# Performance work log

Measured on AMD Instinct MI355X. Metric: run time of the kernel, lower is better.

## Reference

```python
import jax, jax.numpy as jnp
import numpy as np

HIDDEN = 1024
N_HEADS = 16
N_LAYERS = 10
LOCAL_K = 3
TOKEN_T, TOKEN_H, TOKEN_W = 4, 16, 16
PATCH_SIZE = 2
LATENT_C = 16
TOKEN_DIM = LATENT_C * PATCH_SIZE * PATCH_SIZE  # 64
TOKEN_IN = TOKEN_DIM + 1                        # 65
N_TOKENS = TOKEN_T * TOKEN_H * TOKEN_W          # 1024
B = 1
HEAD_DIM = HIDDEN // N_HEADS
LN_EPS = 1e-5


def layer_norm(x, w, b):
    m = x.mean(-1, keepdims=True)
    v = ((x - m) ** 2).mean(-1, keepdims=True)
    return (x - m) * jax.lax.rsqrt(v + LN_EPS) * w + b


def patchify(lat):
    Bx, T, C, H, W = lat.shape
    ph, pw = H // PATCH_SIZE, W // PATCH_SIZE
    x = lat.reshape(Bx, T, C, ph, PATCH_SIZE, pw, PATCH_SIZE)
    x = x.transpose(0, 1, 3, 5, 2, 4, 6)
    return x.reshape(Bx, T * ph * pw, C * PATCH_SIZE * PATCH_SIZE)


def unpatchify(tok):
    Bx = tok.shape[0]
    C = TOKEN_DIM // (PATCH_SIZE * PATCH_SIZE)
    x = tok.reshape(Bx, TOKEN_T, TOKEN_H, TOKEN_W, C, PATCH_SIZE, PATCH_SIZE)
    x = x.transpose(0, 1, 4, 2, 5, 3, 6)
    return x.reshape(Bx, TOKEN_T, C, TOKEN_H * PATCH_SIZE, TOKEN_W * PATCH_SIZE)


def gather_neighbors(kv):
    # kv: (B, N, 2D) -> (B, N, 27, 2D), 3x3x3 zero-padded neighborhoods
    Bx, Nx, D2 = kv.shape
    pad = LOCAL_K // 2
    x = kv.reshape(Bx, TOKEN_T, TOKEN_H, TOKEN_W, D2)
    x = jnp.pad(x, ((0, 0), (pad, pad), (pad, pad), (pad, pad), (0, 0)))
    sl = [x[:, dt:dt + TOKEN_T, dh:dh + TOKEN_H, dw:dw + TOKEN_W]
          for dt in range(LOCAL_K) for dh in range(LOCAL_K) for dw in range(LOCAL_K)]
    nb = jnp.stack(sl, axis=4)  # (B,T,H,W,27,2D)
    return nb.reshape(Bx, Nx, LOCAL_K ** 3, D2)


def local_attention(x, qkv_w, out_w):
    Bx, Nx, D = x.shape
    H, d = N_HEADS, HEAD_DIM
    qkv = x @ qkv_w                       # (B,N,3D)
    q, k, v = jnp.split(qkv, 3, axis=-1)
    kv_nb = gather_neighbors(jnp.concatenate([k, v], axis=-1))  # (B,N,27,2D)
    k_nb, v_nb = jnp.split(kv_nb, 2, axis=-1)
    q = q.reshape(Bx, Nx, H, d)
    k_nb = k_nb.reshape(Bx, Nx, LOCAL_K ** 3, H, d)
    v_nb = v_nb.reshape(Bx, Nx, LOCAL_K ** 3, H, d)
    scores = jnp.einsum('bnhd,bnkhd->bnhk', q, k_nb) / np.sqrt(d).astype(np.float32)
    probs = jax.nn.softmax(scores, axis=-1)
    out = jnp.einsum('bnhk,bnkhd->bnhd', probs, v_nb).reshape(Bx, Nx, D)
    return out @ out_w


def global_attention(x, mask_flat, qkv_w, out_w):
    # Each masked query attends to all N keys; math identical to the
    # gather/SDPA/scatter in the original (per-query attention is independent),
    # realized as full attention masked to zero at unmasked positions.
    Bx, Nx, D = x.shape
    H, d = N_HEADS, HEAD_DIM
    qkv = x @ qkv_w
    q, k, v = jnp.split(qkv, 3, axis=-1)
    q = q.reshape(Bx, Nx, H, d)
    k = k.reshape(Bx, Nx, H, d)
    v = v.reshape(Bx, Nx, H, d)
    scores = jnp.einsum('bqhd,bkhd->bhqk', q, k) / np.sqrt(d).astype(np.float32)
    probs = jax.nn.softmax(scores, axis=-1)
    out = jnp.einsum('bhqk,bkhd->bqhd', probs, v).reshape(Bx, Nx, D)
    out = out @ out_w
    return out * mask_flat[..., None].astype(out.dtype)


def setup_inputs() -> dict:
    key = jax.random.key(0)
    ks = jax.random.split(key, 24)
    s = 0.02
    L, D = N_LAYERS, HIDDEN
    inp = {
        'latents': jax.random.normal(ks[0], (B, TOKEN_T, LATENT_C, TOKEN_H * PATCH_SIZE, TOKEN_W * PATCH_SIZE), jnp.float32),
        'token_mask': jax.random.uniform(ks[1], (B, TOKEN_T, TOKEN_H, TOKEN_W)) < 0.1,
        'input_proj_w': jax.random.normal(ks[2], (TOKEN_IN, D), jnp.float32) * s,
        'input_proj_b': jnp.zeros((D,), jnp.float32),
        'emb_t': jax.random.normal(ks[3], (TOKEN_T, D), jnp.float32) * s,
        'emb_h': jax.random.normal(ks[4], (TOKEN_H, D), jnp.float32) * s,
        'emb_w': jax.random.normal(ks[5], (TOKEN_W, D), jnp.float32) * s,
        'ln_local_w': jnp.ones((L, D), jnp.float32),
        'ln_local_b': jnp.zeros((L, D), jnp.float32),
        'ln_global_w': jnp.ones((L, D), jnp.float32),
        'ln_global_b': jnp.zeros((L, D), jnp.float32),
        'ln_ffn_w': jnp.ones((L, D), jnp.float32),
        'ln_ffn_b': jnp.zeros((L, D), jnp.float32),
        'local_qkv_w': jax.random.normal(ks[6], (L, D, 3 * D), jnp.float32) * s,
        'local_out_w': jax.random.normal(ks[7], (L, D, D), jnp.float32) * s,
        'global_qkv_w': jax.random.normal(ks[8], (L, D, 3 * D), jnp.float32) * s,
        'global_out_w': jax.random.normal(ks[9], (L, D, D), jnp.float32) * s,
        'ffn_w1': jax.random.normal(ks[10], (L, D, 4 * D), jnp.float32) * s,
        'ffn_b1': jnp.zeros((L, 4 * D), jnp.float32),
        'ffn_w2': jax.random.normal(ks[11], (L, 4 * D, D), jnp.float32) * s,
        'ffn_b2': jnp.zeros((L, D), jnp.float32),
        'final_ln_w': jnp.ones((D,), jnp.float32),
        'final_ln_b': jnp.zeros((D,), jnp.float32),
        # original zero-inits output_proj; use small random so the test is non-trivial
        'out_proj_w': jax.random.normal(ks[12], (D, TOKEN_DIM), jnp.float32) * s,
        'out_proj_b': jnp.zeros((TOKEN_DIM,), jnp.float32),
    }
    return inp


def reference(latents, token_mask, input_proj_w, input_proj_b, emb_t, emb_h, emb_w,
              ln_local_w, ln_local_b, ln_global_w, ln_global_b, ln_ffn_w, ln_ffn_b,
              local_qkv_w, local_out_w, global_qkv_w, global_out_w,
              ffn_w1, ffn_b1, ffn_w2, ffn_b2, final_ln_w, final_ln_b,
              out_proj_w, out_proj_b):
    Bx = latents.shape[0]
    mask_flat = token_mask.reshape(Bx, -1)
    tokens = patchify(latents)                       # (B, N, TOKEN_DIM)
    flag = mask_flat[..., None].astype(tokens.dtype)
    x = jnp.concatenate([tokens, flag], axis=-1) @ input_proj_w + input_proj_b

    tt, hh, ww = jnp.meshgrid(jnp.arange(TOKEN_T), jnp.arange(TOKEN_H), jnp.arange(TOKEN_W), indexing='ij')
    pos = emb_t[tt.reshape(-1)] + emb_h[hh.reshape(-1)] + emb_w[ww.reshape(-1)]
    x = x + pos[None]

    for l in range(N_LAYERS):
        x = x + local_attention(layer_norm(x, ln_local_w[l], ln_local_b[l]), local_qkv_w[l], local_out_w[l])
        x = x + global_attention(layer_norm(x, ln_global_w[l], ln_global_b[l]), mask_flat, global_qkv_w[l], global_out_w[l])
        h = layer_norm(x, ln_ffn_w[l], ln_ffn_b[l])
        h = jax.nn.gelu(h @ ffn_w1[l] + ffn_b1[l], approximate=False) @ ffn_w2[l] + ffn_b2[l]
        x = x + h

    delta = layer_norm(x, final_ln_w, final_ln_b) @ out_proj_w + out_proj_b
    return unpatchify(tokens + delta)
```

## Files before the change

### kernel.cpp

```cpp
#include <hip/hip_runtime.h>
#include <hip/hip_bf16.h>
#include <math.h>

typedef __bf16 bf16;
typedef __bf16 bf16x8 __attribute__((ext_vector_type(8)));
typedef __bf16 bf16x4 __attribute__((ext_vector_type(4)));
typedef float  f32x4 __attribute__((ext_vector_type(4)));
typedef unsigned int u32x4 __attribute__((ext_vector_type(4)));

#define NTOK 1024
#define HID  1024
#define NL   10
#define QCMAX 256

#define EPI_F32   0
#define EPI_GELU  1
#define EPI_RESID 2
#define EPI_BF16  3

__global__ __launch_bounds__(256)
void wtransall_k(const float* __restrict__ lqkv, const float* __restrict__ lout,
                 const float* __restrict__ gqkv, const float* __restrict__ gout,
                 const float* __restrict__ w1,   const float* __restrict__ w2,
                 bf16* __restrict__ lqkvT, bf16* __restrict__ loutT,
                 bf16* __restrict__ gqkvT, bf16* __restrict__ goutT,
                 bf16* __restrict__ w1T,   bf16* __restrict__ w2T)
{
    __shared__ bf16 tile[64 * 64];
    const int b = blockIdx.x;
    const float* W; bf16* O; int K, N, ti;
    if      (b < 768)  { W = lqkv; O = lqkvT; K = 1024; N = 3072; ti = b; }
    else if (b < 1024) { W = lout; O = loutT; K = 1024; N = 1024; ti = b - 768; }
    else if (b < 1792) { W = gqkv; O = gqkvT; K = 1024; N = 3072; ti = b - 1024; }
    else if (b < 2048) { W = gout; O = goutT; K = 1024; N = 1024; ti = b - 1792; }
    else if (b < 3072) { W = w1;   O = w1T;   K = 1024; N = 4096; ti = b - 2048; }
    else               { W = w2;   O = w2T;   K = 4096; N = 1024; ti = b - 3072; }
    const int ntx = N >> 6;
    const int n0 = (ti % ntx) * 64, k0 = (ti / ntx) * 64;
    const long mofs = (long)blockIdx.z * K * N;
    const float* Ws = W + mofs;
    bf16* Wo = O + mofs;
    const int t = threadIdx.x;
    {
        const int r = t >> 2, cc = (t & 3) * 16;
        const int x = (r >> 3) & 7;
        const int g0 = cc >> 3;
        const float* src = Ws + (long)(k0 + r) * N + n0 + cc;
        f32x4 a0 = *(const f32x4*)(src);
        f32x4 a1 = *(const f32x4*)(src + 4);
        f32x4 a2 = *(const f32x4*)(src + 8);
        f32x4 a3 = *(const f32x4*)(src + 12);
        bf16x8 w0, w1v;
        w0[0]=(bf16)a0.x; w0[1]=(bf16)a0.y; w0[2]=(bf16)a0.z; w0[3]=(bf16)a0.w;
        w0[4]=(bf16)a1.x; w0[5]=(bf16)a1.y; w0[6]=(bf16)a1.z; w0[7]=(bf16)a1.w;
        w1v[0]=(bf16)a2.x; w1v[1]=(bf16)a2.y; w1v[2]=(bf16)a2.z; w1v[3]=(bf16)a2.w;
        w1v[4]=(bf16)a3.x; w1v[5]=(bf16)a3.y; w1v[6]=(bf16)a3.z; w1v[7]=(bf16)a3.w;
        *(bf16x8*)&tile[r * 64 + ((g0    ) ^ x) * 8] = w0;
        *(bf16x8*)&tile[r * 64 + ((g0 | 1) ^ x) * 8] = w1v;
    }
    __syncthreads();
    {
        const int n = t >> 2, kc = (t & 3) * 16;
        const int g = n >> 3, no = n & 7;
        bf16x8 o0, o1;
#pragma unroll
        for (int j = 0; j < 8; ++j) {
            int r0 = kc + j, r1 = kc + 8 + j;
            o0[j] = tile[r0 * 64 + ((g ^ ((r0 >> 3) & 7)) * 8) + no];
            o1[j] = tile[r1 * 64 + ((g ^ ((r1 >> 3) & 7)) * 8) + no];
        }
        bf16* dst = Wo + (long)(n0 + n) * K + k0 + kc;
        *(bf16x8*)dst = o0;
        *(bf16x8*)(dst + 8) = o1;
    }
}

template<int EPI, int BM, int BN, int KSPLIT>
__global__ __launch_bounds__(256)
void gemm_k(const bf16* __restrict__ A, int lda, long bsA,
            const bf16* __restrict__ Bt, int ldb, long bsB,
            void* __restrict__ Cv, int ldc, long bsC,
            const float* __restrict__ bias, int K)
{
    constexpr int WC  = (BM == 128) ? 2 : 4;
    constexpr int WTN = BN / WC;
    constexpr int NF  = WTN / 16;
    __shared__ bf16 Al[2][BM * 32];
    __shared__ bf16 Bl[2][BN * 32];

    const int t    = threadIdx.x;
    const int lane = t & 63;
    const int wv   = t >> 6;
    const int wr   = wv / WC, wc = wv % WC;
    const int lrow = lane & 15, lk = lane >> 4;
    const int n0   = blockIdx.x * BN;
    const int m0   = blockIdx.y * BM;
    const int ks   = (KSPLIT > 1) ? (blockIdx.z % KSPLIT) : 0;
    const int bz   = (KSPLIT > 1) ? (blockIdx.z / KSPLIT) : blockIdx.z;
    const int Kc   = K / KSPLIT;

    const bf16* Ab = A  + bsA * bz + (long)ks * Kc;
    const bf16* Bb = Bt + bsB * bz + (long)ks * Kc;

    f32x4 acc[4][NF];
#pragma unroll
    for (int m = 0; m < 4; ++m)
#pragma unroll
        for (int n = 0; n < NF; ++n) acc[m][n] = f32x4{0.f, 0.f, 0.f, 0.f};

    const int sr = t >> 2, sc = (t & 3) * 8;

    auto stage = [&](int buf, int kk) {
#pragma unroll
        for (int i = 0; i < BM / 64; ++i)
            __builtin_amdgcn_global_load_lds(
                (const __attribute__((address_space(1))) void*)(Ab + (long)(m0 + sr + i * 64) * lda + kk + sc),
                (__attribute__((address_space(3))) void*)(&Al[buf][i * 2048 + t * 8]), 16, 0, 0);
#pragma unroll
        for (int i = 0; i < BN / 64; ++i)
            __builtin_amdgcn_global_load_lds(
                (const __attribute__((address_space(1))) void*)(Bb + (long)(n0 + sr + i * 64) * ldb + kk + sc),
                (__attribute__((address_space(3))) void*)(&Bl[buf][i * 2048 + t * 8]), 16, 0, 0);
    };

    stage(0, 0);
    __syncthreads();
    int cur = 0;
    for (int k0 = 0; k0 < Kc; k0 += 32) {
        if (k0 + 32 < Kc) stage(cur ^ 1, k0 + 32);
        bf16x8 af[4], bfv[NF];
#pragma unroll
        for (int m = 0; m < 4; ++m)
            af[m] = *(const bf16x8*)&Al[cur][(wr * 64 + m * 16 + lrow) * 32 + lk * 8];
#pragma unroll
        for (int n = 0; n < NF; ++n)
            bfv[n] = *(const bf16x8*)&Bl[cur][(wc * WTN + n * 16 + lrow) * 32 + lk * 8];
#pragma unroll
        for (int m = 0; m < 4; ++m)
#pragma unroll
            for (int n = 0; n < NF; ++n)
                acc[m][n] = __builtin_amdgcn_mfma_f32_16x16x32_bf16(af[m], bfv[n], acc[m][n], 0, 0, 0);
        __syncthreads();
        cur ^= 1;
    }

    float* Cf = (float*)Cv + bsC * blockIdx.z;
    bf16*  Cb = (bf16*)Cv + bsC * blockIdx.z;
#pragma unroll
    for (int m = 0; m < 4; ++m)
#pragma unroll
        for (int n = 0; n < NF; ++n) {
            const int c = n0 + wc * WTN + n * 16 + lrow;
#pragma unroll
            for (int q = 0; q < 4; ++q) {
                const int r = m0 + wr * 64 + m * 16 + lk * 4 + q;
                const float v = acc[m][n][q];
                const long off = (long)r * ldc + c;
                if (EPI == EPI_F32)        Cf[off] = v;
                else if (EPI == EPI_BF16)  Cb[off] = (bf16)v;
                else if (EPI == EPI_RESID) Cf[off] += v;
                else {
                    float u = v + bias[c];
                    Cb[off] = (bf16)(0.5f * u * (1.f + erff(u * 0.70710678118654752f)));
                }
            }
        }
}

template<int NS, bool BIAS, bool SCATTER>
__global__ __launch_bounds__(256)
void ln_add_k(float* __restrict__ x, const float* __restrict__ parts, long pstride,
              const float* __restrict__ bias, const int* __restrict__ rmap,
              const float* __restrict__ w, const float* __restrict__ b,
              bf16* __restrict__ o)
{
    int row  = blockIdx.x * 4 + (threadIdx.x >> 6);
    int lane = threadIdx.x & 63;
    f32x4* xr = (f32x4*)(x + (long)row * HID) + lane * 4;
    f32x4 v[4];
#pragma unroll
    for (int i = 0; i < 4; ++i) v[i] = xr[i];

    if (NS > 0) {
        int prow = SCATTER ? rmap[row] : row;
        if (!SCATTER || prow >= 0) {
            const float* pp = parts + (long)prow * 1024 + lane * 16;
#pragma unroll
            for (int ksi = 0; ksi < NS; ++ksi) {
                const f32x4* q = (const f32x4*)(pp + (long)ksi * pstride);
#pragma unroll
                for (int i = 0; i < 4; ++i) v[i] += q[i];
            }
            if (BIAS) {
                const f32x4* bb = (const f32x4*)bias + lane * 4;
#pragma unroll
                for (int i = 0; i < 4; ++i) v[i] += bb[i];
            }
#pragma unroll
            for (int i = 0; i < 4; ++i) xr[i] = v[i];
        }
    }

    float s = 0.f;
#pragma unroll
    for (int i = 0; i < 4; ++i) s += v[i].x + v[i].y + v[i].z + v[i].w;
    for (int m = 32; m; m >>= 1) s += __shfl_xor(s, m);
    float mean = s * (1.f / 1024.f);
    f32x4 d[4];
    float ss = 0.f;
#pragma unroll
    for (int i = 0; i < 4; ++i) {
        d[i] = v[i] - mean;
        ss += d[i].x * d[i].x + d[i].y * d[i].y + d[i].z * d[i].z + d[i].w * d[i].w;
    }
    for (int m = 32; m; m >>= 1) ss += __shfl_xor(ss, m);
    float rs = rsqrtf(ss * (1.f / 1024.f) + 1e-5f);
    const f32x4* wp = (const f32x4*)w + lane * 4;
    const f32x4* bp = (const f32x4*)b + lane * 4;
    bf16x8 o0, o1;
#pragma unroll
    for (int i = 0; i < 4; ++i) {
        f32x4 wv = wp[i], bv = bp[i];
        f32x4 e;
        e.x = d[i].x * rs * wv.x + bv.x; e.y = d[i].y * rs * wv.y + bv.y;
        e.z = d[i].z * rs * wv.z + bv.z; e.w = d[i].w * rs * wv.w + bv.w;
        if (i < 2) { o0[i*4+0]=(bf16)e.x; o0[i*4+1]=(bf16)e.y; o0[i*4+2]=(bf16)e.z; o0[i*4+3]=(bf16)e.w; }
        else       { int k=(i-2)*4; o1[k+0]=(bf16)e.x; o1[k+1]=(bf16)e.y; o1[k+2]=(bf16)e.z; o1[k+3]=(bf16)e.w; }
    }
    bf16* op = o + (long)row * HID + lane * 16;
    *(bf16x8*)op = o0;
    *(bf16x8*)(op + 8) = o1;
}

__global__ __launch_bounds__(256)
void red4pv_k(const float* __restrict__ p, bf16* __restrict__ Oc)
{
    int i = blockIdx.x * 256 + threadIdx.x;
    int d4 = (i & 15) * 4;
    int r  = (i >> 4) & 255;
    int h  = i >> 12;
    const float* base = p + (long)(h * 4) * 16384 + r * 64 + d4;
    f32x4 s = *(const f32x4*)base;
    s += *(const f32x4*)(base + 16384);
    s += *(const f32x4*)(base + 32768);
    s += *(const f32x4*)(base + 49152);
    bf16x4 o;
    o[0] = (bf16)s.x; o[1] = (bf16)s.y; o[2] = (bf16)s.z; o[3] = (bf16)s.w;
    *(bf16x4*)(Oc + (long)r * 1024 + h * 64 + d4) = o;
}

__global__ __launch_bounds__(256)
void lattn_k(const bf16* __restrict__ qkv, bf16* __restrict__ ao)
{
    int w    = blockIdx.x * 4 + (threadIdx.x >> 6);
    int lane = threadIdx.x & 63;
    int n = w >> 4, h = w & 15;
    int tt = n >> 8, hh = (n >> 4) & 15, ww = n & 15;

    int nj = -1;
    float dotv = 0.f;
    if (lane < 27) {
        int dt = lane / 9 - 1, dh = (lane % 9) / 3 - 1, dw = lane % 3 - 1;
        int t2 = tt + dt, h2 = hh + dh, w2 = ww + dw;
        if (t2 >= 0 && t2 < 4 && h2 >= 0 && h2 < 16 && w2 >= 0 && w2 < 16)
            nj = (t2 << 8) | (h2 << 4) | w2;
    }
    if (nj >= 0) {
        const bf16x8* qp = (const bf16x8*)(qkv + (long)n * 3072 + h * 64);
        const bf16x8* kp = (const bf16x8*)(qkv + (long)nj * 3072 + 1024 + h * 64);
#pragma unroll
        for (int i = 0; i < 8; ++i) {
            bf16x8 q8 = qp[i], k8 = kp[i];
#pragma unroll
            for (int j = 0; j < 8; ++j) dotv += (float)q8[j] * (float)k8[j];
        }
    }
    float sc = (lane < 27) ? dotv * 0.125f : -3.0e38f;
    float mx = sc;
    for (int m = 32; m; m >>= 1) mx = fmaxf(mx, __shfl_xor(mx, m));
    float e = (lane < 27) ? __expf(sc - mx) : 0.f;
    float s = e;
    for (int m = 32; m; m >>= 1) s += __shfl_xor(s, m);
    float p = e / s;

    float acc = 0.f;
    for (int j = 0; j < 27; ++j) {
        float pj = __shfl(p, j);
        int  njj = __shfl(nj, j);
        if (njj >= 0) acc += pj * (float)qkv[(long)njj * 3072 + 2048 + h * 64 + lane];
    }
    ao[(long)n * 1024 + h * 64 + lane] = (bf16)acc;
}

__global__ void compact_k(const int* __restrict__ mask, int* __restrict__ qidx,
                          int* __restrict__ rmap)
{
    int lane = threadIdx.x;
    int total = 0;
    for (int base = 0; base < 1024; base += 64) {
        int m = (mask[base + lane] != 0) ? 1 : 0;
        unsigned long long bal = __ballot(m);
        int pos = total + (int)__popcll(bal & ((1ull << lane) - 1ull));
        int ok = (m && pos < QCMAX);
        if (ok) qidx[pos] = base + lane;
        rmap[base + lane] = ok ? pos : -1;
        total += (int)__popcll(bal);
    }
    for (int i = total + lane; i < QCMAX; i += 64) qidx[i] = -1;
}

__global__ __launch_bounds__(256)
void qkvbuild_k(const bf16* __restrict__ qkv, const int* __restrict__ qidx,
                bf16* __restrict__ Qc, bf16* __restrict__ Kh, bf16* __restrict__ Vt)
{
    __shared__ bf16 vt[64][72];
    const int h = blockIdx.y;
    const int t = threadIdx.x;
    if (blockIdx.x < 4) {
        const int r = blockIdx.x * 64 + (t >> 2), dc = (t & 3) * 16;
        const int q = qidx[r];
        bf16x8 o0, o1;
        if (q >= 0) {
            const bf16x8* src = (const bf16x8*)(qkv + (long)q * 3072 + h * 64 + dc);
            bf16x8 a = src[0], b = src[1];
#pragma unroll
            for (int j = 0; j < 8; ++j) {
                o0[j] = (bf16)((float)a[j] * 0.125f);
                o1[j] = (bf16)((float)b[j] * 0.125f);
            }
        } else {
#pragma unroll
            for (int j = 0; j < 8; ++j) { o0[j] = (bf16)0.f; o1[j] = (bf16)0.f; }
        }
        bf16* dst = Qc + (long)h * (QCMAX * 64) + (long)r * 64 + dc;
        *(bf16x8*)dst = o0;
        *(bf16x8*)(dst + 8) = o1;
        return;
    }
    const int k0 = (blockIdx.x - 4) * 64;
    {
        const int r = t >> 2, dc = (t & 3) * 16;
        const bf16x8* kp = (const bf16x8*)(qkv + (long)(k0 + r) * 3072 + 1024 + h * 64 + dc);
        const bf16x8* vp = (const bf16x8*)(qkv + (long)(k0 + r) * 3072 + 2048 + h * 64 + dc);
        bf16x8 k0v = kp[0], k1v = kp[1];
        bf16* kd = Kh + (long)h * (NTOK * 64) + (long)(k0 + r) * 64 + dc;
        *(bf16x8*)kd = k0v;
        *(bf16x8*)(kd + 8) = k1v;
        *(bf16x8*)&vt[r][dc]     = vp[0];
        *(bf16x8*)&vt[r][dc + 8] = vp[1];
    }
    __syncthreads();
    {
        const int d = t >> 2, kc = (t & 3) * 16;
        bf16x8 o0, o1;
#pragma unroll
        for (int j = 0; j < 8; ++j) { o0[j] = vt[kc + j][d]; o1[j] = vt[kc + 8 + j][d]; }
        bf16* dst = Vt + (long)h * (64 * NTOK) + (long)d * NTOK + k0 + kc;
        *(bf16x8*)dst = o0;
        *(bf16x8*)(dst + 8) = o1;
    }
}

__global__ __launch_bounds__(256)
void softmax_k(const float* __restrict__ S, bf16* __restrict__ P)
{
    int row  = blockIdx.x * 4 + (threadIdx.x >> 6);
    int lane = threadIdx.x & 63;
    const f32x4* sp = (const f32x4*)(S + (long)row * 1024) + lane * 4;
    f32x4 v[4];
#pragma unroll
    for (int i = 0; i < 4; ++i) v[i] = sp[i];
    float mx = -3.0e38f;
#pragma unroll
    for (int i = 0; i < 4; ++i)
        mx = fmaxf(mx, fmaxf(fmaxf(v[i].x, v[i].y), fmaxf(v[i].z, v[i].w)));
    for (int m = 32; m; m >>= 1) mx = fmaxf(mx, __shfl_xor(mx, m));
    f32x4 ev[4];
    float sum = 0.f;
#pragma unroll
    for (int i = 0; i < 4; ++i) {
        ev[i].x = __expf(v[i].x - mx); ev[i].y = __expf(v[i].y - mx);
        ev[i].z = __expf(v[i].z - mx); ev[i].w = __expf(v[i].w - mx);
        sum += ev[i].x + ev[i].y + ev[i].z + ev[i].w;
    }
    for (int m = 32; m; m >>= 1) sum += __shfl_xor(sum, m);
    float inv = 1.f / sum;
    bf16x8 o0, o1;
#pragma unroll
    for (int i = 0; i < 4; ++i) {
        f32x4 e = ev[i] * inv;
        if (i < 2) { o0[i*4+0]=(bf16)e.x; o0[i*4+1]=(bf16)e.y; o0[i*4+2]=(bf16)e.z; o0[i*4+3]=(bf16)e.w; }
        else       { int k=(i-2)*4; o1[k+0]=(bf16)e.x; o1[k+1]=(bf16)e.y; o1[k+2]=(bf16)e.z; o1[k+3]=(bf16)e.w; }
    }
    bf16* op = P + (long)row * 1024 + lane * 16;
    *(bf16x8*)op = o0;
    *(bf16x8*)(op + 8) = o1;
}

__global__ __launch_bounds__(256)
void prep_k(const float* __restrict__ lat, const int* __restrict__ mask,
            const float* __restrict__ Wi, const float* __restrict__ bi,
            const float* __restrict__ et, const float* __restrict__ eh,
            const float* __restrict__ ew,
            float* __restrict__ x, float* __restrict__ tokens)
{
    __shared__ float tl[16][65];
    int t = threadIdx.x;
    int n0 = blockIdx.x * 16;
    for (int idx = t; idx < 16 * 65; idx += 256) {
        int ti = idx / 65, d = idx % 65;
        int n = n0 + ti;
        int tt = n >> 8, hh = (n >> 4) & 15, wwi = n & 15;
        float v;
        if (d < 64) {
            int c = d >> 2, ph = (d >> 1) & 1, pw = d & 1;
            v = lat[(((long)tt * 16 + c) * 32 + hh * 2 + ph) * 32 + wwi * 2 + pw];
            tokens[(long)n * 64 + d] = v;
        } else {
            v = mask[n] ? 1.f : 0.f;
        }
        tl[ti][d] = v;
    }
    __syncthreads();
    f32x4 acc[16];
#pragma unroll
    for (int i = 0; i < 16; ++i) acc[i] = f32x4{0.f, 0.f, 0.f, 0.f};
    for (int d = 0; d < 65; ++d) {
        f32x4 wv = *(const f32x4*)(Wi + (long)d * 1024 + t * 4);
#pragma unroll
        for (int ti = 0; ti < 16; ++ti) acc[ti] += tl[ti][d] * wv;
    }
    f32x4 bb = *(const f32x4*)(bi + t * 4);
    for (int ti = 0; ti < 16; ++ti) {
        int n = n0 + ti;
        int tt = n >> 8, hh = (n >> 4) & 15, wwi = n & 15;
        f32x4 pos = *(const f32x4*)(et + (long)tt * 1024 + t * 4)
                  + *(const f32x4*)(eh + (long)hh * 1024 + t * 4)
                  + *(const f32x4*)(ew + (long)wwi * 1024 + t * 4);
        *(f32x4*)(x + (long)n * 1024 + t * 4) = acc[ti] + bb + pos;
    }
}

__global__ __launch_bounds__(256)
void final_k(const bf16* __restrict__ xn, const float* __restrict__ OW,
             const float* __restrict__ ob, const float* __restrict__ tokens,
             float* __restrict__ out)
{
    __shared__ bf16 xl[8][1024];
    __shared__ float part[4][8][64];
    int t = threadIdx.x;
    int n0 = blockIdx.x * 8;
    for (int i = t; i < 1024; i += 256)
        ((u32x4*)xl)[i] = ((const u32x4*)(xn + (long)n0 * 1024))[i];
    __syncthreads();
    int j = t & 63, s = t >> 6;
    float acc[8] = {0.f, 0.f, 0.f, 0.f, 0.f, 0.f, 0.f, 0.f};
    for (int k = s * 256; k < s * 256 + 256; ++k) {
        float w = OW[(long)k * 64 + j];
#pragma unroll
        for (int ti = 0; ti < 8; ++ti) acc[ti] += (float)xl[ti][k] * w;
    }
    for (int ti = 0; ti < 8; ++ti) part[s][ti][j] = acc[ti];
    __syncthreads();
    if (s == 0) {
        for (int ti = 0; ti < 8; ++ti) {
            int n = n0 + ti;
            float v = part[0][ti][j] + part[1][ti][j] + part[2][ti][j] + part[3][ti][j]
                    + ob[j] + tokens[(long)n * 64 + j];
            int tt = n >> 8, hh = (n >> 4) & 15, wwi = n & 15;
            int c = j >> 2, ph = (j >> 1) & 1, pw = j & 1;
            out[(((long)tt * 16 + c) * 32 + hh * 2 + ph) * 32 + wwi * 2 + pw] = v;
        }
    }
}

extern "C" void kernel_launch(void* const* d_in, const int* in_sizes, int n_in,
                              void* d_out, int out_size, void* d_ws, size_t ws_size,
                              hipStream_t stream)
{
    const float* latents = (const float*)d_in[0];
    const int*   mask    = (const int*)d_in[1];
    const float* ipw  = (const float*)d_in[2];
    const float* ipb  = (const float*)d_in[3];
    const float* et   = (const float*)d_in[4];
    const float* eh   = (const float*)d_in[5];
    const float* ew   = (const float*)d_in[6];
    const float* lnlw = (const float*)d_in[7];
    const float* lnlb = (const float*)d_in[8];
    const float* lngw = (const float*)d_in[9];
    const float* lngb = (const float*)d_in[10];
    const float* lnfw = (const float*)d_in[11];
    const float* lnfb = (const float*)d_in[12];
    const float* lqkv = (const float*)d_in[13];
    const float* lout = (const float*)d_in[14];
    const float* gqkv = (const float*)d_in[15];
    const float* gout = (const float*)d_in[16];
    const float* w1   = (const float*)d_in[17];
    const float* b1   = (const float*)d_in[18];
    const float* w2   = (const float*)d_in[19];
    const float* b2   = (const float*)d_in[20];
    const float* flw  = (const float*)d_in[21];
    const float* flb  = (const float*)d_in[22];
    const float* opw  = (const float*)d_in[23];
    const float* opb  = (const float*)d_in[24];

    char* p = (char*)d_ws;
    auto alloc = [&](size_t bytes) { char* r = p; p += (bytes + 255) & ~(size_t)255; return r; };
    float* x      = (float*)alloc((size_t)4 << 20);
    bf16*  xn     = (bf16*)alloc((size_t)2 << 20);
    bf16*  qkvb   = (bf16*)alloc((size_t)6 << 20);
    bf16*  ao     = (bf16*)alloc((size_t)2 << 20);
    bf16*  hbuf   = (bf16*)alloc((size_t)8 << 20);
    float* tokens = (float*)alloc((size_t)256 << 10);
    bf16*  Qc     = (bf16*)alloc((size_t)512 << 10);
    bf16*  Kh     = (bf16*)alloc((size_t)2 << 20);
    bf16*  Vt     = (bf16*)alloc((size_t)2 << 20);
    float* S      = (float*)alloc((size_t)16 << 20);
    bf16*  P      = (bf16*)alloc((size_t)8 << 20);
    bf16*  Oc     = (bf16*)alloc((size_t)512 << 10);
    int*   qidx   = (int*)alloc(4096);
    int*   rmap   = (int*)alloc(4096);
    float* goutp  = (float*)alloc((size_t)8 * 256 * 1024 * 4);
    float* pvp    = (float*)alloc((size_t)64 * 256 * 64 * 4);
    float* f2p    = (float*)alloc((size_t)4 * 1024 * 1024 * 4);
    bf16* lqkvT = (bf16*)alloc((size_t)10 * 3072 * 1024 * 2);
    bf16* loutT = (bf16*)alloc((size_t)10 * 1024 * 1024 * 2);
    bf16* gqkvT = (bf16*)alloc((size_t)10 * 3072 * 1024 * 2);
    bf16* goutT = (bf16*)alloc((size_t)10 * 1024 * 1024 * 2);
    bf16* w1T   = (bf16*)alloc((size_t)10 * 4096 * 1024 * 2);
    bf16* w2T   = (bf16*)alloc((size_t)10 * 1024 * 4096 * 2);

    wtransall_k<<<dim3(4096, 1, NL), 256, 0, stream>>>(
        lqkv, lout, gqkv, gout, w1, w2, lqkvT, loutT, gqkvT, goutT, w1T, w2T);

    prep_k<<<64, 256, 0, stream>>>(latents, mask, ipw, ipb, et, eh, ew, x, tokens);
    compact_k<<<1, 64, 0, stream>>>(mask, qidx, rmap);

    for (int l = 0; l < NL; ++l) {
        const long wq  = (long)l * 3072 * 1024;
        const long wo  = (long)l * 1024 * 1024;
        const long wf1 = (long)l * 4096 * 1024;

        if (l == 0)
            ln_add_k<0, false, false><<<256, 256, 0, stream>>>(
                x, nullptr, 0, nullptr, nullptr, lnlw, lnlb, xn);
        else
            ln_add_k<4, true, false><<<256, 256, 0, stream>>>(
                x, f2p, (long)1024 * 1024, b2 + (l - 1) * 1024, nullptr,
                lnlw + l * HID, lnlb + l * HID, xn);

        gemm_k<EPI_BF16, 64, 128, 1><<<dim3(24, 16, 1), 256, 0, stream>>>(
            xn, 1024, 0, lqkvT + wq, 1024, 0, qkvb, 3072, 0, nullptr, 1024);
        lattn_k<<<4096, 256, 0, stream>>>(qkvb, ao);
        gemm_k<EPI_RESID, 64, 128, 1><<<dim3(8, 16, 1), 256, 0, stream>>>(
            ao, 1024, 0, loutT + wo, 1024, 0, x, 1024, 0, nullptr, 1024);

        ln_add_k<0, false, false><<<256, 256, 0, stream>>>(
            x, nullptr, 0, nullptr, nullptr, lngw + l * HID, lngb + l * HID, xn);

        gemm_k<EPI_BF16, 64, 128, 1><<<dim3(24, 16, 1), 256, 0, stream>>>(
            xn, 1024, 0, gqkvT + wq, 1024, 0, qkvb, 3072, 0, nullptr, 1024);
        qkvbuild_k<<<dim3(20, 16), 256, 0, stream>>>(qkvb, qidx, Qc, Kh, Vt);
        gemm_k<EPI_F32, 64, 128, 1><<<dim3(8, 4, 16), 256, 0, stream>>>(
            Qc, 64, (long)256 * 64, Kh, 64, (long)1024 * 64,
            S, 1024, (long)256 * 1024, nullptr, 64);
        softmax_k<<<1024, 256, 0, stream>>>(S, P);
        gemm_k<EPI_F32, 64, 64, 4><<<dim3(1, 4, 64), 256, 0, stream>>>(
            P, 1024, (long)256 * 1024, Vt, 1024, (long)64 * 1024,
            pvp, 64, (long)256 * 64, nullptr, 1024);
        red4pv_k<<<256, 256, 0, stream>>>(pvp, Oc);
        gemm_k<EPI_F32, 64, 128, 8><<<dim3(8, 4, 8), 256, 0, stream>>>(
            Oc, 1024, 0, goutT + wo, 1024, 0, goutp, 1024, (long)256 * 1024, nullptr, 1024);

        ln_add_k<8, false, true><<<256, 256, 0, stream>>>(
            x, goutp, (long)256 * 1024, nullptr, rmap,
            lnfw + l * HID, lnfb + l * HID, xn);

        gemm_k<EPI_GELU, 64, 128, 1><<<dim3(32, 16, 1), 256, 0, stream>>>(
            xn, 1024, 0, w1T + wf1, 1024, 0, hbuf, 4096, 0, b1 + l * 4096, 1024);
        gemm_k<EPI_F32, 64, 128, 4><<<dim3(8, 16, 4), 256, 0, stream>>>(
            hbuf, 4096, 0, w2T + wf1, 4096, 0, f2p, 1024, (long)1024 * 1024, nullptr, 4096);
    }

    ln_add_k<4, true, false><<<256, 256, 0, stream>>>(
        x, f2p, (long)1024 * 1024, b2 + 9 * 1024, nullptr, flw, flb, xn);
    final_k<<<128, 256, 0, stream>>>(xn, opw, opb, tokens, (float*)d_out);
}
```

Baseline: 2.232 ms.

## Read fp32 weights directly in GEMM, drop upfront weight transpose-convert kernel

Removes the kernel that converted and transposed all layer weights from fp32 to bf16 before the network ran. Each weight GEMM now loads fp32 K-major weight tiles straight into LDS with an XOR swizzle and converts to bf16 while building the MFMA fragments. This avoids one full pass over all weights (read fp32, write bf16) per call, but each GEMM now moves twice the weight bytes, uses twice the B-tile LDS, and does scalar strided LDS reads plus conversions in the inner loop.

```diff
diff --git a/kernel.cpp b/kernel.cpp
--- a/kernel.cpp
+++ b/kernel.cpp
@@ -18,75 +18,20 @@
 #define EPI_RESID 2
 #define EPI_BF16  3
 
-__global__ __launch_bounds__(256)
-void wtransall_k(const float* __restrict__ lqkv, const float* __restrict__ lout,
-                 const float* __restrict__ gqkv, const float* __restrict__ gout,
-                 const float* __restrict__ w1,   const float* __restrict__ w2,
-                 bf16* __restrict__ lqkvT, bf16* __restrict__ loutT,
-                 bf16* __restrict__ gqkvT, bf16* __restrict__ goutT,
-                 bf16* __restrict__ w1T,   bf16* __restrict__ w2T)
-{
-    __shared__ bf16 tile[64 * 64];
-    const int b = blockIdx.x;
-    const float* W; bf16* O; int K, N, ti;
-    if      (b < 768)  { W = lqkv; O = lqkvT; K = 1024; N = 3072; ti = b; }
-    else if (b < 1024) { W = lout; O = loutT; K = 1024; N = 1024; ti = b - 768; }
-    else if (b < 1792) { W = gqkv; O = gqkvT; K = 1024; N = 3072; ti = b - 1024; }
-    else if (b < 2048) { W = gout; O = goutT; K = 1024; N = 1024; ti = b - 1792; }
-    else if (b < 3072) { W = w1;   O = w1T;   K = 1024; N = 4096; ti = b - 2048; }
-    else               { W = w2;   O = w2T;   K = 4096; N = 1024; ti = b - 3072; }
-    const int ntx = N >> 6;
-    const int n0 = (ti % ntx) * 64, k0 = (ti / ntx) * 64;
-    const long mofs = (long)blockIdx.z * K * N;
-    const float* Ws = W + mofs;
-    bf16* Wo = O + mofs;
-    const int t = threadIdx.x;
-    {
-        const int r = t >> 2, cc = (t & 3) * 16;
-        const int x = (r >> 3) & 7;
-        const int g0 = cc >> 3;
-        const float* src = Ws + (long)(k0 + r) * N + n0 + cc;
-        f32x4 a0 = *(const f32x4*)(src);
-        f32x4 a1 = *(const f32x4*)(src + 4);
-        f32x4 a2 = *(const f32x4*)(src + 8);
-        f32x4 a3 = *(const f32x4*)(src + 12);
-        bf16x8 w0, w1v;
-        w0[0]=(bf16)a0.x; w0[1]=(bf16)a0.y; w0[2]=(bf16)a0.z; w0[3]=(bf16)a0.w;
-        w0[4]=(bf16)a1.x; w0[5]=(bf16)a1.y; w0[6]=(bf16)a1.z; w0[7]=(bf16)a1.w;
-        w1v[0]=(bf16)a2.x; w1v[1]=(bf16)a2.y; w1v[2]=(bf16)a2.z; w1v[3]=(bf16)a2.w;
-        w1v[4]=(bf16)a3.x; w1v[5]=(bf16)a3.y; w1v[6]=(bf16)a3.z; w1v[7]=(bf16)a3.w;
-        *(bf16x8*)&tile[r * 64 + ((g0    ) ^ x) * 8] = w0;
-        *(bf16x8*)&tile[r * 64 + ((g0 | 1) ^ x) * 8] = w1v;
-    }
-    __syncthreads();
-    {
-        const int n = t >> 2, kc = (t & 3) * 16;
-        const int g = n >> 3, no = n & 7;
-        bf16x8 o0, o1;
-#pragma unroll
-        for (int j = 0; j < 8; ++j) {
-            int r0 = kc + j, r1 = kc + 8 + j;
-            o0[j] = tile[r0 * 64 + ((g ^ ((r0 >> 3) & 7)) * 8) + no];
-            o1[j] = tile[r1 * 64 + ((g ^ ((r1 >> 3) & 7)) * 8) + no];
-        }
-        bf16* dst = Wo + (long)(n0 + n) * K + k0 + kc;
-        *(bf16x8*)dst = o0;
-        *(bf16x8*)(dst + 8) = o1;
-    }
-}
-
-template<int EPI, int BM, int BN, int KSPLIT>
+template<int EPI, int BM, int BN, int KSPLIT, bool BF32>
 __global__ __launch_bounds__(256)
 void gemm_k(const bf16* __restrict__ A, int lda, long bsA,
-            const bf16* __restrict__ Bt, int ldb, long bsB,
+            const void* __restrict__ Bv, int ldb, long bsB,
             void* __restrict__ Cv, int ldc, long bsC,
             const float* __restrict__ bias, int K)
 {
+    static_assert(!BF32 || BN == 128, "f32 B-path assumes BN=128");
     constexpr int WC  = (BM == 128) ? 2 : 4;
     constexpr int WTN = BN / WC;
     constexpr int NF  = WTN / 16;
     __shared__ bf16 Al[2][BM * 32];
-    __shared__ bf16 Bl[2][BN * 32];
+    constexpr int BLBYTES = BF32 ? (2 * 32 * BN * 4) : (2 * BN * 32 * 2);
+    __shared__ __align__(16) char Bl_raw[BLBYTES];
 
     const int t    = threadIdx.x;
     const int lane = t & 63;
@@ -99,8 +44,9 @@
     const int bz   = (KSPLIT > 1) ? (blockIdx.z / KSPLIT) : blockIdx.z;
     const int Kc   = K / KSPLIT;
 
-    const bf16* Ab = A  + bsA * bz + (long)ks * Kc;
-    const bf16* Bb = Bt + bsB * bz + (long)ks * Kc;
+    const bf16*  Ab  = A + bsA * bz + (long)ks * Kc;
+    const bf16*  Bbh = BF32 ? nullptr : ((const bf16*)Bv + bsB * bz + (long)ks * Kc);
+    const float* Bbf = BF32 ? ((const float*)Bv + bsB * bz + (long)ks * Kc * ldb) : nullptr;
 
     f32x4 acc[4][NF];
 #pragma unroll
@@ -116,11 +62,25 @@
             __builtin_amdgcn_global_load_lds(
                 (const __attribute__((address_space(1))) void*)(Ab + (long)(m0 + sr + i * 64) * lda + kk + sc),
                 (__attribute__((address_space(3))) void*)(&Al[buf][i * 2048 + t * 8]), 16, 0, 0);
-#pragma unroll
-        for (int i = 0; i < BN / 64; ++i)
-            __builtin_amdgcn_global_load_lds(
-                (const __attribute__((address_space(1))) void*)(Bb + (long)(n0 + sr + i * 64) * ldb + kk + sc),
-                (__attribute__((address_space(3))) void*)(&Bl[buf][i * 2048 + t * 8]), 16, 0, 0);
+        if (BF32) {
+            float* Blf = (float*)Bl_raw + buf * (32 * BN);
+            const int g = t & 31, r8 = t >> 5;
+#pragma unroll
+            for (int i = 0; i < 4; ++i) {
+                const float* src = Bbf + (long)(kk + i * 8 + r8) * ldb + n0
+                                 + ((((g >> 2) ^ (i & 3)) << 4) | ((g & 3) << 2));
+                __builtin_amdgcn_global_load_lds(
+                    (const __attribute__((address_space(1))) void*)src,
+                    (__attribute__((address_space(3))) void*)(Blf + i * 1024 + t * 4), 16, 0, 0);
+            }
+        } else {
+            bf16* Blh = (bf16*)Bl_raw + buf * (BN * 32);
+#pragma unroll
+            for (int i = 0; i < BN / 64; ++i)
+                __builtin_amdgcn_global_load_lds(
+                    (const __attribute__((address_space(1))) void*)(Bbh + (long)(n0 + sr + i * 64) * ldb + kk + sc),
+                    (__attribute__((address_space(3))) void*)(Blh + i * 2048 + t * 8), 16, 0, 0);
+        }
     };
 
     stage(0, 0);
@@ -132,9 +92,24 @@
 #pragma unroll
         for (int m = 0; m < 4; ++m)
             af[m] = *(const bf16x8*)&Al[cur][(wr * 64 + m * 16 + lrow) * 32 + lk * 8];
-#pragma unroll
-        for (int n = 0; n < NF; ++n)
-            bfv[n] = *(const bf16x8*)&Bl[cur][(wc * WTN + n * 16 + lrow) * 32 + lk * 8];
+        if (BF32) {
+            const float* Bf = (const float*)Bl_raw + cur * (32 * BN);
+            const int cb = (wc * WTN) >> 4;
+#pragma unroll
+            for (int n = 0; n < NF; ++n) {
+                const int c16 = (((cb + n) ^ lk) << 4) + lrow;
+                bf16x8 bb;
+#pragma unroll
+                for (int j = 0; j < 8; ++j)
+                    bb[j] = (bf16)Bf[(lk * 8 + j) * BN + c16];
+                bfv[n] = bb;
+            }
+        } else {
+            const bf16* Bh = (const bf16*)Bl_raw + cur * (BN * 32);
+#pragma unroll
+            for (int n = 0; n < NF; ++n)
+                bfv[n] = *(const bf16x8*)&Bh[(wc * WTN + n * 16 + lrow) * 32 + lk * 8];
+        }
 #pragma unroll
         for (int m = 0; m < 4; ++m)
 #pragma unroll
@@ -523,23 +498,17 @@
     float* goutp  = (float*)alloc((size_t)8 * 256 * 1024 * 4);
     float* pvp    = (float*)alloc((size_t)64 * 256 * 64 * 4);
     float* f2p    = (float*)alloc((size_t)4 * 1024 * 1024 * 4);
-    bf16* lqkvT = (bf16*)alloc((size_t)10 * 3072 * 1024 * 2);
-    bf16* loutT = (bf16*)alloc((size_t)10 * 1024 * 1024 * 2);
-    bf16* gqkvT = (bf16*)alloc((size_t)10 * 3072 * 1024 * 2);
-    bf16* goutT = (bf16*)alloc((size_t)10 * 1024 * 1024 * 2);
-    bf16* w1T   = (bf16*)alloc((size_t)10 * 4096 * 1024 * 2);
-    bf16* w2T   = (bf16*)alloc((size_t)10 * 1024 * 4096 * 2);
-
-    wtransall_k<<<dim3(4096, 1, NL), 256, 0, stream>>>(
-        lqkv, lout, gqkv, gout, w1, w2, lqkvT, loutT, gqkvT, goutT, w1T, w2T);
 
     prep_k<<<64, 256, 0, stream>>>(latents, mask, ipw, ipb, et, eh, ew, x, tokens);
     compact_k<<<1, 64, 0, stream>>>(mask, qidx, rmap);
 
     for (int l = 0; l < NL; ++l) {
-        const long wq  = (long)l * 3072 * 1024;
-        const long wo  = (long)l * 1024 * 1024;
-        const long wf1 = (long)l * 4096 * 1024;
+        const float* lqkv_l = lqkv + (long)l * 1024 * 3072;
+        const float* lout_l = lout + (long)l * 1024 * 1024;
+        const float* gqkv_l = gqkv + (long)l * 1024 * 3072;
+        const float* gout_l = gout + (long)l * 1024 * 1024;
+        const float* w1_l   = w1   + (long)l * 1024 * 4096;
+        const float* w2_l   = w2   + (long)l * 4096 * 1024;
 
         if (l == 0)
             ln_add_k<0, false, false><<<256, 256, 0, stream>>>(
@@ -549,37 +518,37 @@
                 x, f2p, (long)1024 * 1024, b2 + (l - 1) * 1024, nullptr,
                 lnlw + l * HID, lnlb + l * HID, xn);
 
-        gemm_k<EPI_BF16, 64, 128, 1><<<dim3(24, 16, 1), 256, 0, stream>>>(
-            xn, 1024, 0, lqkvT + wq, 1024, 0, qkvb, 3072, 0, nullptr, 1024);
+        gemm_k<EPI_BF16, 64, 128, 1, true><<<dim3(24, 16, 1), 256, 0, stream>>>(
+            xn, 1024, 0, lqkv_l, 3072, 0, qkvb, 3072, 0, nullptr, 1024);
         lattn_k<<<4096, 256, 0, stream>>>(qkvb, ao);
-        gemm_k<EPI_RESID, 64, 128, 1><<<dim3(8, 16, 1), 256, 0, stream>>>(
-            ao, 1024, 0, loutT + wo, 1024, 0, x, 1024, 0, nullptr, 1024);
+        gemm_k<EPI_RESID, 64, 128, 1, true><<<dim3(8, 16, 1), 256, 0, stream>>>(
+            ao, 1024, 0, lout_l, 1024, 0, x, 1024, 0, nullptr, 1024);
 
         ln_add_k<0, false, false><<<256, 256, 0, stream>>>(
             x, nullptr, 0, nullptr, nullptr, lngw + l * HID, lngb + l * HID, xn);
 
-        gemm_k<EPI_BF16, 64, 128, 1><<<dim3(24, 16, 1), 256, 0, stream>>>(
-            xn, 1024, 0, gqkvT + wq, 1024, 0, qkvb, 3072, 0, nullptr, 1024);
+        gemm_k<EPI_BF16, 64, 128, 1, true><<<dim3(24, 16, 1), 256, 0, stream>>>(
+            xn, 1024, 0, gqkv_l, 3072, 0, qkvb, 3072, 0, nullptr, 1024);
         qkvbuild_k<<<dim3(20, 16), 256, 0, stream>>>(qkvb, qidx, Qc, Kh, Vt);
-        gemm_k<EPI_F32, 64, 128, 1><<<dim3(8, 4, 16), 256, 0, stream>>>(
+        gemm_k<EPI_F32, 64, 128, 1, false><<<dim3(8, 4, 16), 256, 0, stream>>>(
             Qc, 64, (long)256 * 64, Kh, 64, (long)1024 * 64,
             S, 1024, (long)256 * 1024, nullptr, 64);
         softmax_k<<<1024, 256, 0, stream>>>(S, P);
-        gemm_k<EPI_F32, 64, 64, 4><<<dim3(1, 4, 64), 256, 0, stream>>>(
+        gemm_k<EPI_F32, 64, 64, 4, false><<<dim3(1, 4, 64), 256, 0, stream>>>(
             P, 1024, (long)256 * 1024, Vt, 1024, (long)64 * 1024,
             pvp, 64, (long)256 * 64, nullptr, 1024);
         red4pv_k<<<256, 256, 0, stream>>>(pvp, Oc);
-        gemm_k<EPI_F32, 64, 128, 8><<<dim3(8, 4, 8), 256, 0, stream>>>(
-            Oc, 1024, 0, goutT + wo, 1024, 0, goutp, 1024, (long)256 * 1024, nullptr, 1024);
+        gemm_k<EPI_F32, 64, 128, 8, true><<<dim3(8, 4, 8), 256, 0, stream>>>(
+            Oc, 1024, 0, gout_l, 1024, 0, goutp, 1024, (long)256 * 1024, nullptr, 1024);
 
         ln_add_k<8, false, true><<<256, 256, 0, stream>>>(
             x, goutp, (long)256 * 1024, nullptr, rmap,
             lnfw + l * HID, lnfb + l * HID, xn);
 
-        gemm_k<EPI_GELU, 64, 128, 1><<<dim3(32, 16, 1), 256, 0, stream>>>(
-            xn, 1024, 0, w1T + wf1, 1024, 0, hbuf, 4096, 0, b1 + l * 4096, 1024);
-        gemm_k<EPI_F32, 64, 128, 4><<<dim3(8, 16, 4), 256, 0, stream>>>(
-            hbuf, 4096, 0, w2T + wf1, 4096, 0, f2p, 1024, (long)1024 * 1024, nullptr, 4096);
+        gemm_k<EPI_GELU, 64, 128, 1, true><<<dim3(32, 16, 1), 256, 0, stream>>>(
+            xn, 1024, 0, w1_l, 4096, 0, hbuf, 4096, 0, b1 + l * 4096, 1024);
+        gemm_k<EPI_F32, 64, 128, 4, true><<<dim3(8, 16, 4), 256, 0, stream>>>(
+            hbuf, 4096, 0, w2_l, 1024, 0, f2p, 1024, (long)1024 * 1024, nullptr, 4096);
     }
 
     ln_add_k<4, true, false><<<256, 256, 0, stream>>>(
```

New measurement: 2.588 ms. 1.16x slower.

## Deepen GEMM prefetch to two stages and drop split-K for PV

Applied to the files above, without the earlier changes.

The GEMM main loop now issues loads two K-steps ahead, with explicit vmcnt waits and raw barriers instead of __syncthreads after each stage, so global-to-LDS copies overlap more with MFMA work. Separately, the P·V GEMM no longer uses split-K with a float partial buffer and a reduction kernel. It writes bf16 directly into the concatenated head output, which removes one launch and a round-trip of partials through memory. The cost is fewer blocks for the PV GEMM (64 down to 16 in z) and fragile hand-written waitcnt counts that must match the number of loads issued per stage.

```diff
diff --git a/kernel.cpp b/kernel.cpp
--- a/kernel.cpp
+++ b/kernel.cpp
@@ -85,6 +85,7 @@
     constexpr int WC  = (BM == 128) ? 2 : 4;
     constexpr int WTN = BN / WC;
     constexpr int NF  = WTN / 16;
+    constexpr int NLD = BM / 64 + BN / 64;
     __shared__ bf16 Al[2][BM * 32];
     __shared__ bf16 Bl[2][BN * 32];
 
@@ -123,11 +124,20 @@
                 (__attribute__((address_space(3))) void*)(&Bl[buf][i * 2048 + t * 8]), 16, 0, 0);
     };
 
+    const int nsteps = Kc >> 5;
     stage(0, 0);
-    __syncthreads();
+    if (nsteps > 1) stage(1, 32);
     int cur = 0;
-    for (int k0 = 0; k0 < Kc; k0 += 32) {
-        if (k0 + 32 < Kc) stage(cur ^ 1, k0 + 32);
+    for (int i = 0; i < nsteps; ++i) {
+        if (i + 1 < nsteps) {
+            if constexpr (NLD == 2)      asm volatile("s_waitcnt vmcnt(2)" ::: "memory");
+            else if constexpr (NLD == 3) asm volatile("s_waitcnt vmcnt(3)" ::: "memory");
+            else                         asm volatile("s_waitcnt vmcnt(4)" ::: "memory");
+        } else {
+            asm volatile("s_waitcnt vmcnt(0)" ::: "memory");
+        }
+        __builtin_amdgcn_s_barrier();
+
         bf16x8 af[4], bfv[NF];
 #pragma unroll
         for (int m = 0; m < 4; ++m)
@@ -140,7 +150,9 @@
 #pragma unroll
             for (int n = 0; n < NF; ++n)
                 acc[m][n] = __builtin_amdgcn_mfma_f32_16x16x32_bf16(af[m], bfv[n], acc[m][n], 0, 0, 0);
-        __syncthreads();
+
+        __builtin_amdgcn_s_barrier();
+        if (i + 2 < nsteps) stage(cur, (i + 2) * 32);
         cur ^= 1;
     }
 
@@ -230,23 +242,6 @@
     bf16* op = o + (long)row * HID + lane * 16;
     *(bf16x8*)op = o0;
     *(bf16x8*)(op + 8) = o1;
-}
-
-__global__ __launch_bounds__(256)
-void red4pv_k(const float* __restrict__ p, bf16* __restrict__ Oc)
-{
-    int i = blockIdx.x * 256 + threadIdx.x;
-    int d4 = (i & 15) * 4;
-    int r  = (i >> 4) & 255;
-    int h  = i >> 12;
-    const float* base = p + (long)(h * 4) * 16384 + r * 64 + d4;
-    f32x4 s = *(const f32x4*)base;
-    s += *(const f32x4*)(base + 16384);
-    s += *(const f32x4*)(base + 32768);
-    s += *(const f32x4*)(base + 49152);
-    bf16x4 o;
-    o[0] = (bf16)s.x; o[1] = (bf16)s.y; o[2] = (bf16)s.z; o[3] = (bf16)s.w;
-    *(bf16x4*)(Oc + (long)r * 1024 + h * 64 + d4) = o;
 }
 
 __global__ __launch_bounds__(256)
@@ -521,7 +516,6 @@
     int*   qidx   = (int*)alloc(4096);
     int*   rmap   = (int*)alloc(4096);
     float* goutp  = (float*)alloc((size_t)8 * 256 * 1024 * 4);
-    float* pvp    = (float*)alloc((size_t)64 * 256 * 64 * 4);
     float* f2p    = (float*)alloc((size_t)4 * 1024 * 1024 * 4);
     bf16* lqkvT = (bf16*)alloc((size_t)10 * 3072 * 1024 * 2);
     bf16* loutT = (bf16*)alloc((size_t)10 * 1024 * 1024 * 2);
@@ -565,10 +559,9 @@
             Qc, 64, (long)256 * 64, Kh, 64, (long)1024 * 64,
             S, 1024, (long)256 * 1024, nullptr, 64);
         softmax_k<<<1024, 256, 0, stream>>>(S, P);
-        gemm_k<EPI_F32, 64, 64, 4><<<dim3(1, 4, 64), 256, 0, stream>>>(
+        gemm_k<EPI_BF16, 64, 64, 1><<<dim3(1, 4, 16), 256, 0, stream>>>(
             P, 1024, (long)256 * 1024, Vt, 1024, (long)64 * 1024,
-            pvp, 64, (long)256 * 64, nullptr, 1024);
-        red4pv_k<<<256, 256, 0, stream>>>(pvp, Oc);
+            Oc, 1024, 64, nullptr, 1024);
         gemm_k<EPI_F32, 64, 128, 8><<<dim3(8, 4, 8), 256, 0, stream>>>(
             Oc, 1024, 0, goutT + wo, 1024, 0, goutp, 1024, (long)256 * 1024, nullptr, 1024);
 
```

Result: faster. 2.164 ms (median of 3 runs) (-3.0%).
